# Kernel optimization log

Measured on AMD Instinct MI355X. Metric: run time of the kernel, lower is better.

Reference implementation:

```python
import jax, jax.numpy as jnp
from jax import lax
import numpy as np

K = 2000      # self.k: entries kept per sample
T_SC = 3      # number of IHT iterations
DN = ('NCHW', 'OIHW', 'NCHW')


def keep_k_largest(X, k):
    # Per-sample hard threshold: keep the k largest-magnitude entries of the
    # flattened [C,H,W] activations, zero the rest (exactly k kept, as in argsort).
    B = X.shape[0]
    flat = X.reshape(B, -1)                                # [B, N]
    _, idx = lax.top_k(jnp.abs(flat), k)                   # [B, k]
    vals = jnp.take_along_axis(flat, idx, axis=1)          # [B, k]
    out = jnp.zeros_like(flat).at[jnp.arange(B)[:, None], idx].set(vals)
    return out.reshape(X.shape)


def _D_apply(X, W_D):
    # ConvTranspose2d(numb_atom -> dp_channels), stride 1, no padding:
    # full correlation with the spatially flipped, io-swapped kernel.
    kh, kw = W_D.shape[2], W_D.shape[3]
    Wt = jnp.flip(jnp.transpose(W_D, (1, 0, 2, 3)), (2, 3))  # [dp, atoms, kh, kw]
    return lax.conv_general_dilated(X, Wt, (1, 1),
                                    [(kh - 1, kh - 1), (kw - 1, kw - 1)],
                                    dimension_numbers=DN)


def _Dt_apply(Z, W_D):
    # Conv2d(dp_channels -> numb_atom) VALID; D_trans.weight = D.weight.permute(0,1,3,2)
    Wt = jnp.transpose(W_D, (0, 1, 3, 2))                  # [atoms, dp, kh, kw]
    return lax.conv_general_dilated(Z, Wt, (1, 1), 'VALID', dimension_numbers=DN)


def setup_inputs() -> dict:
    key = jax.random.key(0)
    k1, k2, k3 = jax.random.split(key, 3)
    Y = jax.random.normal(k1, (32, 3, 64, 64), jnp.float32)
    X0 = jax.random.normal(k2, (32, 128, 57, 57), jnp.float32)   # random init X in forward
    W_D = jax.random.normal(k3, (128, 3, 8, 8), jnp.float32) * 0.05
    return {"Y": Y, "X0": X0, "W_D": W_D}


def reference(Y, X0, W_D):
    # HT_arg = X - D_trans(D(X) - Y); then T_SC hard-threshold iterations.
    HT_arg = X0 - _Dt_apply(_D_apply(X0, W_D) - Y, W_D)
    X = HT_arg
    for i in range(T_SC):
        X = keep_k_largest(HT_arg, K)
        if i < T_SC - 1:  # final HT_arg update in the original is unused
            HT_arg = X - _Dt_apply(_D_apply(X, W_D) - Y, W_D)
    return X
```

## Files before the change

### kernel.cpp

```cpp
#include <hip/hip_runtime.h>

#define BATCH 32
#define ATOMS 128
#define CCH 3
#define XH 57
#define XW 57
#define OHH 64
#define OWW 64
#define KSEL 2000
#define PIX (XH*XW)
#define NPS (ATOMS*PIX)
#define NTOT (BATCH*NPS)
#define RPS (CCH*OHH*OWW)
#define RTOT (BATCH*RPS)
#define CANDCAP 32768
#define NW 24576
#define ZWORDS (32*2048*2 + 32)

__global__ __launch_bounds__(256) void prep_k(const float* __restrict__ Wg,
    double* __restrict__ WDd, float* __restrict__ Wt2f,
    const float* __restrict__ Y, double* __restrict__ Rd,
    unsigned* __restrict__ zbuf) {
  int e = blockIdx.x * 256 + threadIdx.x;
  if (e < NW) {
    {
      int kw = e & 7; int t = e >> 3; int c = t % 3; t /= 3; int kh = t & 7; int a = t >> 3;
      WDd[e] = (double)Wg[(a*3 + c)*64 + kh*8 + kw];
    }
    {
      int a = e & 127; int t = e >> 7; int j = t & 7; int i = (t >> 3) & 7; int c = t >> 6;
      Wt2f[e] = Wg[(a*3 + c)*64 + j*8 + i];
    }
  }
  if (e < RTOT) Rd[e] = -(double)Y[e];
  if (e < ZWORDS) zbuf[e] = 0;
}

__global__ __launch_bounds__(256) void convD_k(const float* __restrict__ X,
    const double* __restrict__ WDd, double* __restrict__ Rd) {
  __shared__ double Xs[4][11][72];
  int p = blockIdx.x;
  int lg = (p & 7) * 256 + (p >> 3);
  int b = lg >> 6; int rem = lg & 63;
  int band = rem >> 2, quarter = rem & 3;
  int row0 = band * 4;
  int a_base = quarter * 32;
  int tid = threadIdx.x;
  int ox = tid & 63;
  int wv = __builtin_amdgcn_readfirstlane(tid >> 6);
  const float* Xb = X + (size_t)b * NPS;

  double acc[4][3];
#pragma unroll
  for (int ty = 0; ty < 4; ++ty)
#pragma unroll
    for (int c = 0; c < 3; ++c) acc[ty][c] = 0.0;

  for (int ch = 0; ch < 8; ++ch) {
    __syncthreads();
    for (int e = tid; e < 4 * 11 * 72; e += 256) {
      int ai = e / 792; int rem2 = e - ai * 792;
      int r = rem2 / 72; int ss = rem2 - r * 72;
      int gy = row0 - 7 + r;
      int xcol = ss - 7;
      int a = a_base + ch * 4 + ai;
      float v = 0.0f;
      if ((unsigned)xcol < (unsigned)XW && (unsigned)gy < (unsigned)XH)
        v = Xb[a * PIX + gy * XW + xcol];
      Xs[ai][r][ss] = (double)v;
    }
    __syncthreads();
    {
      int a = a_base + ch * 4 + wv;
      const double* Wa = WDd + a * 192;
#pragma unroll
      for (int r = 0; r < 11; ++r) {
        int gy = row0 - 7 + r;
        if ((unsigned)gy >= (unsigned)XH) continue;
        double xd[8];
#pragma unroll
        for (int t = 0; t < 8; ++t) xd[t] = Xs[wv][r][ox + t];
#pragma unroll
        for (int ty = 0; ty < 4; ++ty) {
          int kh = ty + 7 - r;
          if ((unsigned)kh < 8u) {
            const double* Wk = Wa + kh * 24;
#pragma unroll
            for (int kw = 0; kw < 8; ++kw) {
              acc[ty][0] = fma(xd[7 - kw], Wk[kw],      acc[ty][0]);
              acc[ty][1] = fma(xd[7 - kw], Wk[8 + kw],  acc[ty][1]);
              acc[ty][2] = fma(xd[7 - kw], Wk[16 + kw], acc[ty][2]);
            }
          }
        }
      }
    }
  }
#pragma unroll
  for (int ty = 0; ty < 4; ++ty) {
    int oy = row0 + ty;
#pragma unroll
    for (int c = 0; c < 3; ++c)
      atomicAdd(&Rd[((size_t)(b * CCH + c) << 12) + (oy << 6) + ox], acc[ty][c]);
  }
}

__global__ __launch_bounds__(256) void convD_sparse_k(const float* __restrict__ Wg,
    const int* __restrict__ nzidx, const float* __restrict__ nzval,
    const float* __restrict__ Y, float* __restrict__ R) {
  __shared__ double accd[512];
  __shared__ float Wf[8192];
  __shared__ int   li[KSEL];
  __shared__ float lv[KSEL];
  int p = blockIdx.x;
  int lg = (p & 7) * 96 + (p >> 3);
  int s = lg / 24; int r = lg % 24; int c = r >> 3; int band = r & 7;
  int row0 = band * 8;
  int tid = threadIdx.x;
  for (int e = tid; e < 512; e += 256) accd[e] = 0.0;
  for (int e = tid; e < 8192; e += 256) {
    int a = e >> 6, k2 = e & 63;
    Wf[e] = Wg[(a * 3 + c) * 64 + k2];
  }
  for (int e = tid; e < KSEL; e += 256) {
    li[e] = nzidx[s * KSEL + e];
    lv[e] = nzval[s * KSEL + e];
  }
  __syncthreads();
  int slot = tid >> 3, kw = tid & 7;
  for (int e = slot; e < KSEL; e += 32) {
    int idx = li[e];
    int a = (int)((unsigned)idx / 3249u);
    int pp = idx - a * 3249;
    int y = (int)((unsigned)pp / 57u);
    int x = pp - y * 57;
    int dy = y - row0;
    if (dy < -7 || dy > 7) continue;
    double val = (double)lv[e];
    const float* wp = Wf + (a << 6) + kw;
#pragma unroll
    for (int kh = 0; kh < 8; ++kh) {
      int rr = dy + kh;
      if ((unsigned)rr < 8u)
        __hip_atomic_fetch_add(&accd[(rr << 6) + x + kw],
                               val * (double)wp[kh << 3],
                               __ATOMIC_RELAXED, __HIP_MEMORY_SCOPE_WORKGROUP);
    }
  }
  __syncthreads();
  const float* Yb = Y + (((size_t)(s * CCH + c)) << 12) + (row0 << 6);
  float* Rb = R + (((size_t)(s * CCH + c)) << 12) + (row0 << 6);
  for (int e = tid; e < 512; e += 256)
    Rb[e] = (float)(accd[e] - (double)Yb[e]);
}

template <typename TR>
__global__ __launch_bounds__(256) void convDt_k(const TR* __restrict__ R,
    const float* __restrict__ Wt2f, const float* __restrict__ Xprev,
    float* __restrict__ HT, unsigned* __restrict__ g1) {
  __shared__ float Rl[3][15][72];
  __shared__ unsigned hh[1024];
  int p = blockIdx.x;
  int lg = (p & 7) * 512 + (p >> 3);
  int b = lg >> 7; int rem = lg & 127; int ag = rem >> 3; int by = rem & 7;
  int row0 = by * 8;
  int a0 = ag * 8;
  int tid = threadIdx.x;
  for (int e = tid; e < 1024; e += 256) hh[e] = 0;
  for (int e = tid; e < 3 * 15 * 72; e += 256) {
    int c = e / (15 * 72); int r2 = e - c * (15 * 72);
    int rr = r2 / 72; int cc = r2 - rr * 72;
    int gr = row0 + rr;
    float v = 0.0f;
    if (cc < OWW && gr < OHH)
      v = (float)R[((size_t)(b * CCH + c) << 12) + (gr << 6) + cc];
    Rl[c][rr][cc] = v;
  }
  __syncthreads();
  int x = tid & 63, yg = tid >> 6;
  int yb = yg * 2;
  float acc[8][2];
#pragma unroll
  for (int aa = 0; aa < 8; ++aa) { acc[aa][0] = 0.0f; acc[aa][1] = 0.0f; }

#pragma unroll 1
  for (int c = 0; c < 3; ++c) {
#pragma unroll 1
    for (int j = 0; j < 8; ++j) {
      float rw[9];
#pragma unroll
      for (int r = 0; r < 9; ++r) rw[r] = Rl[c][yb + r][x + j];
#pragma unroll
      for (int i = 0; i < 8; ++i) {
        const float* wp = Wt2f + ((c * 8 + i) * 8 + j) * 128 + a0;
#pragma unroll
        for (int aa = 0; aa < 8; ++aa) {
          float w = wp[aa];
          acc[aa][0] = fmaf(rw[i + 0], w, acc[aa][0]);
          acc[aa][1] = fmaf(rw[i + 1], w, acc[aa][1]);
        }
      }
    }
  }
  if (x < XW) {
#pragma unroll
    for (int ty = 0; ty < 2; ++ty) {
      int yy = row0 + yb + ty;
      if (yy < XH) {
#pragma unroll
        for (int aa = 0; aa < 8; ++aa) {
          size_t xo = (size_t)(b * ATOMS + a0 + aa) * PIX + yy * XW + x;
          float fv = Xprev[xo] - acc[aa][ty];
          HT[xo] = fv;
          unsigned u = __float_as_uint(fv) & 0x7fffffffu;
          unsigned bin = u >> 20;
          atomicAdd(&hh[bin >> 1], 1u << ((bin & 1) << 4));
        }
      }
    }
  }
  __syncthreads();
  unsigned* gp = g1 + (size_t)b * 2048;
  for (int e = tid; e < 1024; e += 256) {
    unsigned v = hh[e];
    unsigned lo = v & 0xffffu, hi = v >> 16;
    if (lo) atomicAdd(&gp[2 * e], lo);
    if (hi) atomicAdd(&gp[2 * e + 1], hi);
  }
}

__global__ __launch_bounds__(256) void histwrite_k(const float* __restrict__ HT,
    const unsigned* __restrict__ g1, int* __restrict__ cand,
    int* __restrict__ candcnt, float* __restrict__ Xo) {
  __shared__ unsigned part[256];
  __shared__ int lidx[4096];
  __shared__ int lcnt, lbase, b1_sh;
  int tid = threadIdx.x;
  int s = blockIdx.x >> 5;
  int chunk = blockIdx.x & 31;
  const unsigned* hg1 = g1 + (size_t)s * 2048;
  unsigned psum = 0;
#pragma unroll
  for (int e = 0; e < 8; ++e) psum += hg1[tid * 8 + e];
  part[tid] = psum;
  if (tid == 0) lcnt = 0;
  __syncthreads();
  if (tid == 0) {
    int Kv = KSEL;
    unsigned cumBefore = 0;
    int bsel = 0;
    for (int q = 255; q >= 0; --q) {
      unsigned ps = part[q];
      if ((int)(cumBefore + ps) >= Kv) {
        for (int e = q * 8 + 7;; --e) {
          unsigned c2 = cumBefore + hg1[e];
          if ((int)c2 >= Kv) { bsel = e; break; }
          cumBefore = c2;
        }
        break;
      }
      cumBefore += ps;
    }
    b1_sh = bsel;
  }
  __syncthreads();
  unsigned blo = (unsigned)(b1_sh > 0 ? b1_sh - 1 : 0);
  size_t sbase = (size_t)s * NPS;
  const uint4* U4 = (const uint4*)(HT + sbase);
  float4* X4 = (float4*)(Xo + sbase);
  for (int i4 = chunk * 256 + tid; i4 < NPS / 4; i4 += 32 * 256) {
    uint4 v = U4[i4];
    unsigned uu[4] = {v.x, v.y, v.z, v.w};
    float oo[4];
#pragma unroll
    for (int t = 0; t < 4; ++t) {
      int il = i4 * 4 + t;
      unsigned u = uu[t] & 0x7fffffffu;
      unsigned bin = u >> 20;
      if (bin >= blo) {
        oo[t] = __uint_as_float(uu[t]);
        int pos = atomicAdd(&lcnt, 1);
        if (pos < 4096) lidx[pos] = il;
      } else {
        oo[t] = 0.0f;
      }
    }
    X4[i4] = make_float4(oo[0], oo[1], oo[2], oo[3]);
  }
  __syncthreads();
  if (tid == 0) {
    int n = lcnt < 4096 ? lcnt : 4096;
    lbase = atomicAdd(&candcnt[s], n);
  }
  __syncthreads();
  int n = lcnt < 4096 ? lcnt : 4096;
  for (int e = tid; e < n; e += 256) {
    int g = lbase + e;
    if (g < CANDCAP) cand[s * CANDCAP + g] = lidx[e];
  }
}

template <typename TR, bool SPX>
__global__ __launch_bounds__(256) void recompute_k(const TR* __restrict__ R,
    const float* __restrict__ Wt2f, const float* __restrict__ X0,
    const int* __restrict__ pnzidx, const float* __restrict__ pnzval,
    const int* __restrict__ cand, const int* __restrict__ candcnt,
    float* __restrict__ candval, unsigned* __restrict__ g1x) {
  __shared__ int hidx[4096];
  __shared__ float hval[4096];
  __shared__ unsigned hx[2048];
  int s = blockIdx.x >> 3;
  int chunk = blockIdx.x & 7;
  int tid = threadIdx.x;
  for (int e = tid; e < 2048; e += 256) hx[e] = 0;
  if constexpr (SPX) {
    for (int e = tid; e < 4096; e += 256) hidx[e] = -1;
    __syncthreads();
    for (int e = tid; e < KSEL; e += 256) {
      int idx = pnzidx[s * KSEL + e];
      float v = pnzval[s * KSEL + e];
      int slot = idx & 4095;
      while (true) {
        int old = atomicCAS(&hidx[slot], -1, idx);
        if (old == -1) { hval[slot] = v; break; }
        slot = (slot + 1) & 4095;
      }
    }
  }
  __syncthreads();
  int n = candcnt[s];
  if (n > CANDCAP) n = CANDCAP;
  const TR* Rb = R + ((size_t)(s * 3) << 12);
  for (int e = chunk * 256 + tid; e < n; e += 2048) {
    int i = cand[s * CANDCAP + e];
    int a = (int)((unsigned)i / 3249u);
    int p = i - a * 3249;
    int y = (int)((unsigned)p / 57u);
    int x = p - y * 57;
    double xprev;
    if constexpr (SPX) {
      xprev = 0.0;
      int slot = i & 4095;
      while (true) {
        int h = hidx[slot];
        if (h == i) { xprev = (double)hval[slot]; break; }
        if (h == -1) break;
        slot = (slot + 1) & 4095;
      }
    } else {
      xprev = (double)X0[(size_t)s * NPS + i];
    }
    double acc = 0.0;
    for (int c = 0; c < 3; ++c) {
#pragma unroll
      for (int ii = 0; ii < 8; ++ii) {
        const TR* rrow = Rb + (c << 12) + ((y + ii) << 6) + x;
        const float* wrow = Wt2f + ((c * 8 + ii) * 8) * 128 + a;
#pragma unroll
        for (int jj = 0; jj < 8; ++jj)
          acc = fma((double)rrow[jj], (double)wrow[jj * 128], acc);
      }
    }
    float cf = (float)(xprev - acc);
    candval[s * CANDCAP + e] = cf;
    unsigned u = __float_as_uint(cf) & 0x7fffffffu;
    atomicAdd(&hx[u >> 20], 1u);
  }
  __syncthreads();
  unsigned* gp = g1x + (size_t)s * 2048;
  for (int e = tid; e < 2048; e += 256)
    if (hx[e]) atomicAdd(&gp[e], hx[e]);
}

__global__ __launch_bounds__(256) void pass3_k(const int* __restrict__ cand,
    int* __restrict__ candcnt, const float* __restrict__ candval,
    unsigned* __restrict__ g1, unsigned* __restrict__ g1x,
    float* __restrict__ Xo, int* __restrict__ nzidx, float* __restrict__ nzval,
    int emit) {
  int s = blockIdx.x;
  __shared__ unsigned h[1024];
  __shared__ unsigned part[256];
  __shared__ int eqidx[1024];
  __shared__ int kidx[2048];
  __shared__ float kval[2048];
  __shared__ int eqn, kcnt;
  __shared__ unsigned tau_sh;
  __shared__ int k3_sh, cutoff_sh, b1_sh, k1_sh, b2_sh, k2_sh;
  int t = threadIdx.x;
  unsigned* hx = g1x + (size_t)s * 2048;
  unsigned s1 = 0;
#pragma unroll
  for (int e = 0; e < 8; ++e) s1 += hx[t * 8 + e];
  part[t] = s1;
  for (int e = t; e < 1024; e += 256) h[e] = 0;
  if (t == 0) { eqn = 0; kcnt = 0; }
  __syncthreads();
  if (t == 0) {
    int Kv = KSEL;
    unsigned cumBefore = 0;
    int bsel = 0;
    for (int q = 255; q >= 0; --q) {
      unsigned ps = part[q];
      if ((int)(cumBefore + ps) >= Kv) {
        for (int e = q * 8 + 7;; --e) {
          unsigned c2 = cumBefore + hx[e];
          if ((int)c2 >= Kv) { bsel = e; break; }
          cumBefore = c2;
        }
        break;
      }
      cumBefore += ps;
    }
    b1_sh = bsel;
    k1_sh = KSEL - (int)cumBefore;
  }
  __syncthreads();
  int n = candcnt[s];
  if (n > CANDCAP) n = CANDCAP;
  const int* cs = cand + s * CANDCAP;
  const float* cv = candval + s * CANDCAP;
  unsigned b1x = (unsigned)b1_sh;
  for (int e = t; e < n; e += 256) {
    unsigned u = __float_as_uint(cv[e]) & 0x7fffffffu;
    if ((u >> 20) == b1x) atomicAdd(&h[(u >> 10) & 1023], 1u);
  }
  __syncthreads();
  part[t] = h[t * 4] + h[t * 4 + 1] + h[t * 4 + 2] + h[t * 4 + 3];
  __syncthreads();
  if (t == 0) {
    int Kv = k1_sh;
    unsigned cumBefore = 0;
    int bsel = 0;
    for (int q = 255; q >= 0; --q) {
      unsigned ps = part[q];
      if ((int)(cumBefore + ps) >= Kv) {
        for (int e = q * 4 + 3;; --e) {
          unsigned c2 = cumBefore + h[e];
          if ((int)c2 >= Kv) { bsel = e; break; }
          cumBefore = c2;
        }
        break;
      }
      cumBefore += ps;
    }
    b2_sh = bsel;
    k2_sh = Kv - (int)cumBefore;
  }
  __syncthreads();
  for (int e = t; e < 1024; e += 256) h[e] = 0;
  __syncthreads();
  unsigned pre21 = (b1x << 10) | (unsigned)b2_sh;
  for (int e = t; e < n; e += 256) {
    unsigned u = __float_as_uint(cv[e]) & 0x7fffffffu;
    if ((u >> 10) == pre21) atomicAdd(&h[u & 1023], 1u);
  }
  __syncthreads();
  if (t == 0) {
    int Kv = k2_sh;
    unsigned cumBefore = 0;
    int b3 = 0;
    for (int e = 1023; e >= 0; --e) {
      unsigned c2 = cumBefore + h[e];
      if ((int)c2 >= Kv) { b3 = e; break; }
      cumBefore = c2;
    }
    tau_sh = (pre21 << 10) | (unsigned)b3;
    k3_sh = Kv - (int)cumBefore;
  }
  __syncthreads();
  unsigned tau = tau_sh;
  for (int e = t; e < n; e += 256) {
    unsigned u = __float_as_uint(cv[e]) & 0x7fffffffu;
    if (u == tau) {
      int pos = atomicAdd(&eqn, 1);
      if (pos < 1024) eqidx[pos] = cs[e];
    }
  }
  __syncthreads();
  if (t == 0) {
    int m = eqn < 1024 ? eqn : 1024;
    int k3 = k3_sh;
    int cutoff;
    if (k3 >= m) {
      cutoff = 0x7fffffff;
    } else {
      int last = -1;
      for (int r = 0; r < k3; ++r) {
        int mn = 0x7fffffff;
        for (int q = 0; q < m; ++q) {
          int v = eqidx[q];
          if (v > last && v < mn) mn = v;
        }
        last = mn;
      }
      cutoff = last;
    }
    cutoff_sh = cutoff;
  }
  __syncthreads();
  int co = cutoff_sh;
  float* Xs = Xo + (size_t)s * NPS;
  for (int e = t; e < n; e += 256) {
    int i = cs[e];
    float cf = cv[e];
    unsigned u = __float_as_uint(cf) & 0x7fffffffu;
    bool keep = (u > tau) || (u == tau && i <= co);
    Xs[i] = keep ? cf : 0.0f;
    if (keep && emit) {
      int pos = atomicAdd(&kcnt, 1);
      if (pos < 2048) { kidx[pos] = i; kval[pos] = cf; }
    }
  }
  __syncthreads();
  if (emit) {
    int kn = kcnt < KSEL ? kcnt : KSEL;
    for (int e = t; e < kn; e += 256) {
      nzidx[s * KSEL + e] = kidx[e];
      nzval[s * KSEL + e] = kval[e];
    }
  }
  unsigned* hg1 = g1 + (size_t)s * 2048;
  for (int e = t; e < 2048; e += 256) { hg1[e] = 0; hx[e] = 0; }
  if (t == 0) candcnt[s] = 0;
}

extern "C" void kernel_launch(void* const* d_in, const int* in_sizes, int n_in,
                              void* d_out, int out_size, void* d_ws, size_t ws_size,
                              hipStream_t stream) {
  const float* Y  = (const float*)d_in[0];
  const float* X0 = (const float*)d_in[1];
  const float* Wg = (const float*)d_in[2];
  float* Xout = (float*)d_out;

  double* WDd  = (double*)d_ws;
  float* Wt2f  = (float*)(WDd + NW);
  float* HT   = Wt2f + NW;
  float* Rbuf = HT + NTOT;
  double* Rd  = (double*)(Rbuf + RTOT);
  unsigned* g1 = (unsigned*)(Rd + RTOT);
  unsigned* g1x = g1 + 32 * 2048;
  int* candcnt = (int*)(g1x + 32 * 2048);
  int* cand = candcnt + 32;
  float* candval = (float*)(cand + 32 * CANDCAP);
  int* nzidx = (int*)(candval + 32 * CANDCAP);
  float* nzval = (float*)(nzidx + 32 * KSEL);

  prep_k<<<dim3((RTOT + 255) / 256), dim3(256), 0, stream>>>(Wg, WDd, Wt2f, Y, Rd, g1);

  for (int it = 0; it < 3; ++it) {
    if (it == 0) {
      convD_k<<<dim3(2048), dim3(256), 0, stream>>>(X0, WDd, Rd);
      convDt_k<double><<<dim3(4096), dim3(256), 0, stream>>>(Rd, Wt2f, X0, HT, g1);
    } else {
      convD_sparse_k<<<dim3(BATCH * CCH * 8), dim3(256), 0, stream>>>(
          Wg, nzidx, nzval, Y, Rbuf);
      convDt_k<float><<<dim3(4096), dim3(256), 0, stream>>>(Rbuf, Wt2f,
          (const float*)Xout, HT, g1);
    }
    histwrite_k<<<dim3(BATCH * 32), dim3(256), 0, stream>>>(
        HT, g1, cand, candcnt, Xout);
    if (it == 0) {
      recompute_k<double, false><<<dim3(BATCH * 8), dim3(256), 0, stream>>>(
          Rd, Wt2f, X0, nullptr, nullptr, cand, candcnt, candval, g1x);
    } else {
      recompute_k<float, true><<<dim3(BATCH * 8), dim3(256), 0, stream>>>(
          Rbuf, Wt2f, X0, nzidx, nzval, cand, candcnt, candval, g1x);
    }
    int emit = (it < 2) ? 1 : 0;
    pass3_k<<<dim3(BATCH), dim3(256), 0, stream>>>(
        cand, candcnt, candval, g1, g1x, Xout, nzidx, nzval, emit);
  }
}
```

Baseline: 1.108 ms.

## Capture previous X in histwrite, drop hash lookup, relayout candidate weights

```diff
diff --git a/kernel.cpp b/kernel.cpp
--- a/kernel.cpp
+++ b/kernel.cpp
@@ -15,12 +15,13 @@
 #define RTOT (BATCH*RPS)
 #define CANDCAP 32768
 #define NW 24576
+#define NWC 32768
 #define ZWORDS (32*2048*2 + 32)
 
 __global__ __launch_bounds__(256) void prep_k(const float* __restrict__ Wg,
     double* __restrict__ WDd, float* __restrict__ Wt2f,
-    const float* __restrict__ Y, double* __restrict__ Rd,
-    unsigned* __restrict__ zbuf) {
+    float* __restrict__ Wcand, const float* __restrict__ Y,
+    double* __restrict__ Rd, unsigned* __restrict__ zbuf) {
   int e = blockIdx.x * 256 + threadIdx.x;
   if (e < NW) {
     {
@@ -31,6 +32,15 @@
       int a = e & 127; int t = e >> 7; int j = t & 7; int i = (t >> 3) & 7; int c = t >> 6;
       Wt2f[e] = Wg[(a*3 + c)*64 + j*8 + i];
     }
+  }
+  if (e < NWC) {
+    int a = e >> 8, r = e & 255;
+    float v = 0.0f;
+    if (r < 192) {
+      int c = r >> 6, ii = (r >> 3) & 7, jj = r & 7;
+      v = Wg[(a*3 + c)*64 + jj*8 + ii];
+    }
+    Wcand[e] = v;
   }
   if (e < RTOT) Rd[e] = -(double)Y[e];
   if (e < ZWORDS) zbuf[e] = 0;
@@ -231,9 +241,11 @@
 
 __global__ __launch_bounds__(256) void histwrite_k(const float* __restrict__ HT,
     const unsigned* __restrict__ g1, int* __restrict__ cand,
-    int* __restrict__ candcnt, float* __restrict__ Xo) {
+    int* __restrict__ candcnt, float* __restrict__ candprev,
+    float* Xo, const float* prevX) {
   __shared__ unsigned part[256];
   __shared__ int lidx[4096];
+  __shared__ float lprev[4096];
   __shared__ int lcnt, lbase, b1_sh;
   int tid = threadIdx.x;
   int s = blockIdx.x >> 5;
@@ -267,10 +279,13 @@
   unsigned blo = (unsigned)(b1_sh > 0 ? b1_sh - 1 : 0);
   size_t sbase = (size_t)s * NPS;
   const uint4* U4 = (const uint4*)(HT + sbase);
+  const float4* P4 = (const float4*)(prevX + sbase);
   float4* X4 = (float4*)(Xo + sbase);
   for (int i4 = chunk * 256 + tid; i4 < NPS / 4; i4 += 32 * 256) {
     uint4 v = U4[i4];
+    float4 pv = P4[i4];
     unsigned uu[4] = {v.x, v.y, v.z, v.w};
+    float pp[4] = {pv.x, pv.y, pv.z, pv.w};
     float oo[4];
 #pragma unroll
     for (int t = 0; t < 4; ++t) {
@@ -280,7 +295,7 @@
       if (bin >= blo) {
         oo[t] = __uint_as_float(uu[t]);
         int pos = atomicAdd(&lcnt, 1);
-        if (pos < 4096) lidx[pos] = il;
+        if (pos < 4096) { lidx[pos] = il; lprev[pos] = pp[t]; }
       } else {
         oo[t] = 0.0f;
       }
@@ -296,69 +311,44 @@
   int n = lcnt < 4096 ? lcnt : 4096;
   for (int e = tid; e < n; e += 256) {
     int g = lbase + e;
-    if (g < CANDCAP) cand[s * CANDCAP + g] = lidx[e];
-  }
-}
-
-template <typename TR, bool SPX>
+    if (g < CANDCAP) {
+      cand[s * CANDCAP + g] = lidx[e];
+      candprev[s * CANDCAP + g] = lprev[e];
+    }
+  }
+}
+
+template <typename TR>
 __global__ __launch_bounds__(256) void recompute_k(const TR* __restrict__ R,
-    const float* __restrict__ Wt2f, const float* __restrict__ X0,
-    const int* __restrict__ pnzidx, const float* __restrict__ pnzval,
-    const int* __restrict__ cand, const int* __restrict__ candcnt,
+    const float* __restrict__ Wcand, const int* __restrict__ cand,
+    const int* __restrict__ candcnt, const float* __restrict__ candprev,
     float* __restrict__ candval, unsigned* __restrict__ g1x) {
-  __shared__ int hidx[4096];
-  __shared__ float hval[4096];
   __shared__ unsigned hx[2048];
-  int s = blockIdx.x >> 3;
-  int chunk = blockIdx.x & 7;
+  int s = blockIdx.x >> 5;
+  int chunk = blockIdx.x & 31;
   int tid = threadIdx.x;
   for (int e = tid; e < 2048; e += 256) hx[e] = 0;
-  if constexpr (SPX) {
-    for (int e = tid; e < 4096; e += 256) hidx[e] = -1;
-    __syncthreads();
-    for (int e = tid; e < KSEL; e += 256) {
-      int idx = pnzidx[s * KSEL + e];
-      float v = pnzval[s * KSEL + e];
-      int slot = idx & 4095;
-      while (true) {
-        int old = atomicCAS(&hidx[slot], -1, idx);
-        if (old == -1) { hval[slot] = v; break; }
-        slot = (slot + 1) & 4095;
-      }
-    }
-  }
   __syncthreads();
   int n = candcnt[s];
   if (n > CANDCAP) n = CANDCAP;
   const TR* Rb = R + ((size_t)(s * 3) << 12);
-  for (int e = chunk * 256 + tid; e < n; e += 2048) {
+  for (int e = chunk * 256 + tid; e < n; e += 32 * 256) {
     int i = cand[s * CANDCAP + e];
     int a = (int)((unsigned)i / 3249u);
     int p = i - a * 3249;
     int y = (int)((unsigned)p / 57u);
     int x = p - y * 57;
-    double xprev;
-    if constexpr (SPX) {
-      xprev = 0.0;
-      int slot = i & 4095;
-      while (true) {
-        int h = hidx[slot];
-        if (h == i) { xprev = (double)hval[slot]; break; }
-        if (h == -1) break;
-        slot = (slot + 1) & 4095;
-      }
-    } else {
-      xprev = (double)X0[(size_t)s * NPS + i];
-    }
+    double xprev = (double)candprev[s * CANDCAP + e];
+    const float* wa = Wcand + (a << 8);
     double acc = 0.0;
     for (int c = 0; c < 3; ++c) {
 #pragma unroll
       for (int ii = 0; ii < 8; ++ii) {
         const TR* rrow = Rb + (c << 12) + ((y + ii) << 6) + x;
-        const float* wrow = Wt2f + ((c * 8 + ii) * 8) * 128 + a;
+        const float* wrow = wa + (c * 8 + ii) * 8;
 #pragma unroll
         for (int jj = 0; jj < 8; ++jj)
-          acc = fma((double)rrow[jj], (double)wrow[jj * 128], acc);
+          acc = fma((double)rrow[jj], (double)wrow[jj], acc);
       }
     }
     float cf = (float)(xprev - acc);
@@ -534,7 +524,8 @@
 
   double* WDd  = (double*)d_ws;
   float* Wt2f  = (float*)(WDd + NW);
-  float* HT   = Wt2f + NW;
+  float* Wcand = Wt2f + NW;
+  float* HT   = Wcand + NWC;
   float* Rbuf = HT + NTOT;
   double* Rd  = (double*)(Rbuf + RTOT);
   unsigned* g1 = (unsigned*)(Rd + RTOT);
@@ -542,10 +533,12 @@
   int* candcnt = (int*)(g1x + 32 * 2048);
   int* cand = candcnt + 32;
   float* candval = (float*)(cand + 32 * CANDCAP);
-  int* nzidx = (int*)(candval + 32 * CANDCAP);
+  float* candprev = candval + 32 * CANDCAP;
+  int* nzidx = (int*)(candprev + 32 * CANDCAP);
   float* nzval = (float*)(nzidx + 32 * KSEL);
 
-  prep_k<<<dim3((RTOT + 255) / 256), dim3(256), 0, stream>>>(Wg, WDd, Wt2f, Y, Rd, g1);
+  prep_k<<<dim3((RTOT + 255) / 256), dim3(256), 0, stream>>>(
+      Wg, WDd, Wt2f, Wcand, Y, Rd, g1);
 
   for (int it = 0; it < 3; ++it) {
     if (it == 0) {
@@ -558,13 +551,13 @@
           (const float*)Xout, HT, g1);
     }
     histwrite_k<<<dim3(BATCH * 32), dim3(256), 0, stream>>>(
-        HT, g1, cand, candcnt, Xout);
+        HT, g1, cand, candcnt, candprev, Xout, (it == 0) ? X0 : (const float*)Xout);
     if (it == 0) {
-      recompute_k<double, false><<<dim3(BATCH * 8), dim3(256), 0, stream>>>(
-          Rd, Wt2f, X0, nullptr, nullptr, cand, candcnt, candval, g1x);
+      recompute_k<double><<<dim3(BATCH * 32), dim3(256), 0, stream>>>(
+          Rd, Wcand, cand, candcnt, candprev, candval, g1x);
     } else {
-      recompute_k<float, true><<<dim3(BATCH * 8), dim3(256), 0, stream>>>(
-          Rbuf, Wt2f, X0, nzidx, nzval, cand, candcnt, candval, g1x);
+      recompute_k<float><<<dim3(BATCH * 32), dim3(256), 0, stream>>>(
+          Rbuf, Wcand, cand, candcnt, candprev, candval, g1x);
     }
     int emit = (it < 2) ? 1 : 0;
     pass3_k<<<dim3(BATCH), dim3(256), 0, stream>>>(
```

After: 955.2 us. 13.8% less time.
